# Optimization experiments

Measured on AMD Instinct MI355X. Metric: run time of the kernel, lower is better.

Reference implementation:

```python
import jax, jax.numpy as jnp
import numpy as np
from jax import lax

B, S, H, W = 64, 256, 512, 512


def _lstm_cell(x_t, h, c, Wih, Whh, bih, bhh):
    # PyTorch LSTMCell gate order: i, f, g, o
    g = x_t @ Wih.T + h @ Whh.T + bih + bhh  # [B, 4H]
    i, f, gg, o = jnp.split(g, 4, axis=-1)
    c_new = jax.nn.sigmoid(f) * c + jax.nn.sigmoid(i) * jnp.tanh(gg)
    h_new = jax.nn.sigmoid(o) * jnp.tanh(c_new)
    return h_new, c_new


def setup_inputs() -> dict:
    key = jax.random.key(0)
    ks = jax.random.split(key, 12)
    bnd = 1.0 / np.sqrt(H)
    u = lambda k, shape, b: jax.random.uniform(k, shape, jnp.float32, -b, b)
    return {
        "x": jax.random.normal(ks[0], (B, S, S), jnp.float32),
        "enc_Wih": u(ks[1], (4 * H, S), bnd),
        "enc_Whh": u(ks[2], (4 * H, H), bnd),
        "enc_bih": u(ks[3], (4 * H,), bnd),
        "enc_bhh": u(ks[4], (4 * H,), bnd),
        "dec_Wih": u(ks[5], (4 * H, S), bnd),
        "dec_Whh": u(ks[6], (4 * H, H), bnd),
        "dec_bih": u(ks[7], (4 * H,), bnd),
        "dec_bhh": u(ks[8], (4 * H,), bnd),
        "w1": u(ks[9], (W, H), 1.0 / np.sqrt(H)),
        "w2": u(ks[10], (W, H), 1.0 / np.sqrt(H)),
        "vt": u(ks[11], (W,), 1.0 / np.sqrt(W)),
    }


def reference(x, enc_Wih, enc_Whh, enc_bih, enc_bhh,
              dec_Wih, dec_Whh, dec_bih, dec_bhh, w1, w2, vt):
    xs = x.transpose(1, 0, 2)  # [S, B, S] time-major

    # ---- encoder LSTM (zero initial state, PyTorch default) ----
    def enc_step(carry, x_t):
        h, c = carry
        h, c = _lstm_cell(x_t, h, c, enc_Wih, enc_Whh, enc_bih, enc_bhh)
        return (h, c), h

    h0 = jnp.zeros((B, H), x.dtype)
    (hT, cT), enc_out = lax.scan(enc_step, (h0, h0), xs)  # enc_out: [S, B, H]

    # loop-invariant W1 projection of encoder outputs
    e1 = jnp.einsum('sbh,wh->sbw', enc_out, w1)  # [S, B, W]

    # ---- decoder: hidden updates each step; cell stays at cT (faithful to source) ----
    def dec_step(h, x_t):
        h_new, _ = _lstm_cell(x_t, h, cT, dec_Wih, dec_Whh, dec_bih, dec_bhh)
        att = jnp.tanh(e1 + (h_new @ w2.T)[None, :, :])   # [S, B, W]
        scores = jnp.einsum('sbw,w->sb', att, vt)          # [S, B]
        lp = jax.nn.log_softmax(scores.T, axis=-1)         # [B, S]
        return h_new, lp

    _, probs = lax.scan(dec_step, hT, xs)  # [S_dec, B, S]
    return probs.transpose(1, 0, 2)        # [B, S_dec, S]
```

## Files before the change

### kernel.cpp

```cpp
#include <hip/hip_runtime.h>
#include <cmath>

__device__ __forceinline__ float sigm(float x) { return 1.0f / (1.0f + __expf(-x)); }

__global__ __launch_bounds__(256) void transpose_w(const float* __restrict__ in,
                                                   float* __restrict__ outT, int K) {
  __shared__ float tile[32][33];
  int tx = threadIdx.x & 31, ty = threadIdx.x >> 5;
  int k0 = blockIdx.x * 32;
  int j0 = blockIdx.y * 32;
#pragma unroll
  for (int i = 0; i < 32; i += 8)
    tile[ty + i][tx] = in[(size_t)(j0 + ty + i) * K + k0 + tx];
  __syncthreads();
#pragma unroll
  for (int i = 0; i < 32; i += 8)
    outT[(size_t)(k0 + ty + i) * 2048 + j0 + tx] = tile[tx][ty + i];
}

__device__ __forceinline__ void gemv_j(const float4* __restrict__ A4,
                                       const float4* __restrict__ W4, int j, int kqx,
                                       int kq, int jlo, int jhi, int b0, int b1,
                                       float (&o0)[8], float (&o1)[8]) {
  int qa = (j << 3) + kqx;
  float4 a04 = A4[b0 * 192 + qa];
  float4 a14 = A4[b1 * 192 + qa];
  int wr = ((j << 3) + kq) << 2;
  float a0v[4] = {a04.x, a04.y, a04.z, a04.w};
  float a1v[4] = {a14.x, a14.y, a14.z, a14.w};
#pragma unroll
  for (int i = 0; i < 4; ++i) {
    float4 wlo = W4[(wr + i) * 8 + jlo];
    float4 whi = W4[(wr + i) * 8 + jhi];
    o0[0] = fmaf(a0v[i], wlo.x, o0[0]);
    o0[1] = fmaf(a0v[i], wlo.y, o0[1]);
    o0[2] = fmaf(a0v[i], wlo.z, o0[2]);
    o0[3] = fmaf(a0v[i], wlo.w, o0[3]);
    o0[4] = fmaf(a0v[i], whi.x, o0[4]);
    o0[5] = fmaf(a0v[i], whi.y, o0[5]);
    o0[6] = fmaf(a0v[i], whi.z, o0[6]);
    o0[7] = fmaf(a0v[i], whi.w, o0[7]);
    o1[0] = fmaf(a1v[i], wlo.x, o1[0]);
    o1[1] = fmaf(a1v[i], wlo.y, o1[1]);
    o1[2] = fmaf(a1v[i], wlo.z, o1[2]);
    o1[3] = fmaf(a1v[i], wlo.w, o1[3]);
    o1[4] = fmaf(a1v[i], whi.x, o1[4]);
    o1[5] = fmaf(a1v[i], whi.y, o1[5]);
    o1[6] = fmaf(a1v[i], whi.z, o1[6]);
    o1[7] = fmaf(a1v[i], whi.w, o1[7]);
  }
}

__global__ __launch_bounds__(256, 1) void lstm_chain(
    const float* __restrict__ WT, const float* __restrict__ x,
    const float* __restrict__ bih, const float* __restrict__ bhh,
    float* __restrict__ HBUF,
    float* __restrict__ Cst,
    unsigned int* __restrict__ flg,
    int is_enc) {
  extern __shared__ float lds[];
  float4* W4 = (float4*)lds;
  float4* A4 = (float4*)(lds + 24576);
  float* gates = lds + 24576 + 12288;
  const int bg = blockIdx.x >> 6, ng = blockIdx.x & 63;
  const int tid = threadIdx.x;
  unsigned int* myflag = flg + (size_t)(bg * 64 + ng) * 32;
  unsigned int* dom = flg + (size_t)bg * 64 * 32;

#pragma unroll
  for (int r = 0; r < 24; ++r) {
    int idx = tid + 256 * r;
    int k = idx >> 3, j = idx & 7;
    float4 v =
        *(const float4*)(WT + (size_t)k * 2048 + (j >> 1) * 512 + ng * 8 + (j & 1) * 4);
    W4[k * 8 + (j ^ ((k >> 2) & 7))] = v;
  }
  float bi_i = 0.f, bi_f = 0.f, bi_g = 0.f, bi_o = 0.f, creg = 0.f;
  if (tid < 128) {
    int b = tid >> 3, n8 = tid & 7;
    int n_g = ng * 8 + n8;
    bi_i = bih[n_g] + bhh[n_g];
    bi_f = bih[512 + n_g] + bhh[512 + n_g];
    bi_g = bih[1024 + n_g] + bhh[1024 + n_g];
    bi_o = bih[1536 + n_g] + bhh[1536 + n_g];
    if (!is_enc) creg = Cst[(size_t)(bg * 16 + b) * 512 + n_g];
  }
#pragma unroll
  for (int r = 0; r < 8; ++r) {
    int idx = tid + 256 * r;
    int b = idx >> 7, q = idx & 127;
    float4 v;
    if (is_enc)
      v = make_float4(0.f, 0.f, 0.f, 0.f);
    else
      v = *(const float4*)(HBUF + ((size_t)(255 * 64) + bg * 16 + b) * 512 + 4 * q);
    A4[b * 192 + (q ^ ((b >> 1) & 7))] = v;
  }
#pragma unroll
  for (int r = 0; r < 4; ++r) {
    int idx = tid + 256 * r;
    int b = idx >> 6, q = idx & 63;
    float4 v = *(const float4*)(x + ((size_t)(bg * 16 + b) * 256 + 0) * 256 + 4 * q);
    A4[b * 192 + ((128 + q) ^ ((b >> 1) & 7))] = v;
  }
  __syncthreads();

  const int w = tid >> 6;
  const int lane = tid & 63;
  const int kq = lane >> 3, b8 = lane & 7;
  const int b0 = 2 * b8, b1 = b0 + 1;
  const int jlo = (2 * w) ^ kq, jhi = (2 * w + 1) ^ kq;
  const int kqx = kq ^ b8;

  for (int t = 0; t < 256; ++t) {
    float acc0[8], acc1[8];
#pragma unroll
    for (int g = 0; g < 8; ++g) { acc0[g] = 0.f; acc1[g] = 0.f; }
#pragma unroll 2
    for (int j = 0; j < 24; ++j)
      gemv_j(A4, W4, j, kqx, kq, jlo, jhi, b0, b1, acc0, acc1);
#pragma unroll
    for (int d = 8; d <= 32; d <<= 1) {
#pragma unroll
      for (int g = 0; g < 8; ++g) {
        acc0[g] += __shfl_xor(acc0[g], d, 64);
        acc1[g] += __shfl_xor(acc1[g], d, 64);
      }
    }
    if (kq == 0) {
#pragma unroll
      for (int g = 0; g < 8; ++g) {
        gates[b0 * 40 + w * 8 + g] = acc0[g];
        gates[b1 * 40 + w * 8 + g] = acc1[g];
      }
    }
    __syncthreads();
    if (tid < 128) {
      int b = tid >> 3, n8 = tid & 7;
      float pi = gates[b * 40 + n8] + bi_i;
      float pf = gates[b * 40 + 8 + n8] + bi_f;
      float pg = gates[b * 40 + 16 + n8] + bi_g;
      float po = gates[b * 40 + 24 + n8] + bi_o;
      float ig = sigm(pi), fg = sigm(pf), gg = tanhf(pg), og = sigm(po);
      float cn = fmaf(fg, creg, ig * gg);
      if (is_enc) creg = cn;
      float hn = og * tanhf(cn);
      float* hp = HBUF + ((size_t)t * 64 + bg * 16 + b) * 512 + ng * 8 + n8;
      __hip_atomic_store(hp, hn, __ATOMIC_RELAXED, __HIP_MEMORY_SCOPE_AGENT);
      if (is_enc && t == 255) Cst[(size_t)(bg * 16 + b) * 512 + ng * 8 + n8] = cn;
    }
    if (t == 255) break;
    asm volatile("s_waitcnt vmcnt(0)" ::: "memory");
    __syncthreads();
    if (tid == 0)
      __hip_atomic_store(myflag, (unsigned)(t + 1), __ATOMIC_RELAXED,
                         __HIP_MEMORY_SCOPE_AGENT);
    asm volatile("" ::: "memory");
#pragma unroll
    for (int r = 0; r < 4; ++r) {
      int idx = tid + 256 * r;
      int b = idx >> 6, q = idx & 63;
      float4 v =
          *(const float4*)(x + ((size_t)(bg * 16 + b) * 256 + (t + 1)) * 256 + 4 * q);
      A4[b * 192 + ((128 + q) ^ ((b >> 1) & 7))] = v;
    }
    if (tid < 64) {
      const unsigned tgt = (unsigned)(t + 1);
      unsigned int* fp = dom + (size_t)tid * 32;
      while (true) {
        unsigned v = __hip_atomic_load(fp, __ATOMIC_RELAXED, __HIP_MEMORY_SCOPE_AGENT);
        if (__all((int)(v >= tgt))) break;
        __builtin_amdgcn_s_sleep(1);
      }
    }
    __syncthreads();
    const float4* hb = (const float4*)(HBUF + (size_t)t * 64 * 512);
#pragma unroll
    for (int r = 0; r < 8; ++r) {
      int idx = tid + 256 * r;
      int b = idx >> 7, q = idx & 127;
      float4 v = hb[(size_t)(bg * 16 + b) * 128 + q];
      A4[b * 192 + (q ^ ((b >> 1) & 7))] = v;
    }
    __syncthreads();
  }
}

typedef __attribute__((ext_vector_type(8))) short bf16x8_t;
typedef __attribute__((ext_vector_type(4))) float f32x4_t;

__device__ __forceinline__ unsigned int pack_bf16_rne(float f0, float f1) {
  unsigned int u0 = __float_as_uint(f0);
  unsigned int u1 = __float_as_uint(f1);
  u0 = (u0 + 0x7FFFu + ((u0 >> 16) & 1u)) >> 16;
  u1 = (u1 + 0x7FFFu + ((u1 >> 16) & 1u)) >> 16;
  return u0 | (u1 << 16);
}

__global__ __launch_bounds__(256) void gemm_bf16(const float* __restrict__ A,
                                                 const float* __restrict__ W,
                                                 float* __restrict__ C) {
  __shared__ unsigned short As[128 * 40];
  __shared__ unsigned short Ws[128 * 40];
  int tid = threadIdx.x;
  int n0 = blockIdx.x * 128, m0 = blockIdx.y * 128;
  int wid = tid >> 6, lane = tid & 63;
  int wr = (wid >> 1) * 64, wc = (wid & 1) * 64;
  int l15 = lane & 15, lk = lane >> 4;
  int srow = tid >> 1, shalf = (tid & 1) * 16;
  f32x4_t acc[4][4];
#pragma unroll
  for (int i = 0; i < 4; ++i)
#pragma unroll
    for (int j = 0; j < 4; ++j) acc[i][j] = (f32x4_t){0.f, 0.f, 0.f, 0.f};

  const float* ap = A + (size_t)(m0 + srow) * 512 + shalf;
  const float* wp = W + (size_t)(n0 + srow) * 512 + shalf;

  for (int k0 = 0; k0 < 512; k0 += 32) {
    float4 av0 = *(const float4*)(ap + k0);
    float4 av1 = *(const float4*)(ap + k0 + 4);
    float4 av2 = *(const float4*)(ap + k0 + 8);
    float4 av3 = *(const float4*)(ap + k0 + 12);
    float4 wv0 = *(const float4*)(wp + k0);
    float4 wv1 = *(const float4*)(wp + k0 + 4);
    float4 wv2 = *(const float4*)(wp + k0 + 8);
    float4 wv3 = *(const float4*)(wp + k0 + 12);
    __syncthreads();
    {
      uint4 pa0, pa1, pw0, pw1;
      pa0.x = pack_bf16_rne(av0.x, av0.y);
      pa0.y = pack_bf16_rne(av0.z, av0.w);
      pa0.z = pack_bf16_rne(av1.x, av1.y);
      pa0.w = pack_bf16_rne(av1.z, av1.w);
      pa1.x = pack_bf16_rne(av2.x, av2.y);
      pa1.y = pack_bf16_rne(av2.z, av2.w);
      pa1.z = pack_bf16_rne(av3.x, av3.y);
      pa1.w = pack_bf16_rne(av3.z, av3.w);
      pw0.x = pack_bf16_rne(wv0.x, wv0.y);
      pw0.y = pack_bf16_rne(wv0.z, wv0.w);
      pw0.z = pack_bf16_rne(wv1.x, wv1.y);
      pw0.w = pack_bf16_rne(wv1.z, wv1.w);
      pw1.x = pack_bf16_rne(wv2.x, wv2.y);
      pw1.y = pack_bf16_rne(wv2.z, wv2.w);
      pw1.z = pack_bf16_rne(wv3.x, wv3.y);
      pw1.w = pack_bf16_rne(wv3.z, wv3.w);
      *(uint4*)&As[srow * 40 + shalf] = pa0;
      *(uint4*)&As[srow * 40 + shalf + 8] = pa1;
      *(uint4*)&Ws[srow * 40 + shalf] = pw0;
      *(uint4*)&Ws[srow * 40 + shalf + 8] = pw1;
    }
    __syncthreads();
    bf16x8_t af[4], bf[4];
#pragma unroll
    for (int mi = 0; mi < 4; ++mi)
      af[mi] = *(const bf16x8_t*)&As[(wr + mi * 16 + l15) * 40 + lk * 8];
#pragma unroll
    for (int ni = 0; ni < 4; ++ni)
      bf[ni] = *(const bf16x8_t*)&Ws[(wc + ni * 16 + l15) * 40 + lk * 8];
#pragma unroll
    for (int mi = 0; mi < 4; ++mi)
#pragma unroll
      for (int ni = 0; ni < 4; ++ni)
        acc[mi][ni] = __builtin_amdgcn_mfma_f32_16x16x32_bf16(af[mi], bf[ni],
                                                              acc[mi][ni], 0, 0, 0);
  }
#pragma unroll
  for (int mi = 0; mi < 4; ++mi)
#pragma unroll
    for (int ni = 0; ni < 4; ++ni) {
      float* cp = C + (size_t)(m0 + wr + mi * 16 + lk * 4) * 512 + n0 + wc + ni * 16 + l15;
#pragma unroll
      for (int r = 0; r < 4; ++r) cp[(size_t)r * 512] = acc[mi][ni][r];
    }
}

__global__ __launch_bounds__(256) void scorer(const float* __restrict__ E1,
                                              const float* __restrict__ H2,
                                              const float* __restrict__ vt,
                                              float* __restrict__ out) {
  extern __shared__ float smem[];
  float* e1s = smem;
  float* h2s = smem + 8256;
  const float k2log2e = 2.885390081777927f;
  int tid = threadIdx.x;
  int sx = blockIdx.x;
  int b = blockIdx.y;
#pragma unroll
  for (int j = 0; j < 8; ++j) {
    int idx = tid + 256 * j;
    int r = idx >> 7, c4 = idx & 127;
    float4 v = *(const float4*)(E1 + ((size_t)(sx * 16 + r) * 64 + b) * 512 + c4 * 4);
    *(float4*)&e1s[r * 516 + c4 * 4] = v;
  }
  int tl = tid >> 4, sl = tid & 15;
  for (int tt = 0; tt < 16; ++tt) {
    __syncthreads();
#pragma unroll
    for (int j = 0; j < 8; ++j) {
      int idx = tid + 256 * j;
      int r = idx >> 7, c4 = idx & 127;
      float4 v = *(const float4*)(H2 + ((size_t)(tt * 16 + r) * 64 + b) * 512 + c4 * 4);
      *(float4*)&h2s[r * 516 + c4 * 4] = v;
    }
    __syncthreads();
    float acc = 0.f;
    const float* ep = &e1s[sl * 516];
    const float* hp = &h2s[tl * 516];
#pragma unroll 8
    for (int w4 = 0; w4 < 128; ++w4) {
      float4 a = *(const float4*)(ep + w4 * 4);
      float4 h = *(const float4*)(hp + w4 * 4);
      float4 vv = *(const float4*)(vt + w4 * 4);
      float x0 = a.x + h.x, x1 = a.y + h.y, x2 = a.z + h.z, x3 = a.w + h.w;
      float t0 = fmaf(-2.f, __builtin_amdgcn_rcpf(__builtin_amdgcn_exp2f(x0 * k2log2e) + 1.f), 1.f);
      float t1 = fmaf(-2.f, __builtin_amdgcn_rcpf(__builtin_amdgcn_exp2f(x1 * k2log2e) + 1.f), 1.f);
      float t2 = fmaf(-2.f, __builtin_amdgcn_rcpf(__builtin_amdgcn_exp2f(x2 * k2log2e) + 1.f), 1.f);
      float t3 = fmaf(-2.f, __builtin_amdgcn_rcpf(__builtin_amdgcn_exp2f(x3 * k2log2e) + 1.f), 1.f);
      acc = fmaf(t0, vv.x, acc);
      acc = fmaf(t1, vv.y, acc);
      acc = fmaf(t2, vv.z, acc);
      acc = fmaf(t3, vv.w, acc);
    }
    out[((size_t)b * 256 + tt * 16 + tl) * 256 + sx * 16 + sl] = acc;
  }
}

__global__ __launch_bounds__(256) void logsoftmax_kernel(float* __restrict__ out) {
  __shared__ float red[8];
  int tid = threadIdx.x;
  int wv = tid >> 6, ln = tid & 63;
  float* row = out + (size_t)blockIdx.x * 256;
  float v = row[tid];
  float m = v;
#pragma unroll
  for (int d = 1; d <= 32; d <<= 1) m = fmaxf(m, __shfl_xor(m, d, 64));
  if (ln == 0) red[wv] = m;
  __syncthreads();
  float mx = fmaxf(fmaxf(red[0], red[1]), fmaxf(red[2], red[3]));
  float e = __expf(v - mx);
  float s = e;
#pragma unroll
  for (int d = 1; d <= 32; d <<= 1) s += __shfl_xor(s, d, 64);
  if (ln == 0) red[4 + wv] = s;
  __syncthreads();
  float lse = logf((red[4] + red[5]) + (red[6] + red[7]));
  row[tid] = v - mx - lse;
}

extern "C" void kernel_launch(void* const* d_in, const int* in_sizes, int n_in,
                              void* d_out, int out_size, void* d_ws, size_t ws_size,
                              hipStream_t stream) {
  (void)in_sizes; (void)n_in; (void)out_size; (void)ws_size;
  const float* x = (const float*)d_in[0];
  const float* eWih = (const float*)d_in[1];
  const float* eWhh = (const float*)d_in[2];
  const float* ebih = (const float*)d_in[3];
  const float* ebhh = (const float*)d_in[4];
  const float* dWih = (const float*)d_in[5];
  const float* dWhh = (const float*)d_in[6];
  const float* dbih = (const float*)d_in[7];
  const float* dbhh = (const float*)d_in[8];
  const float* w1 = (const float*)d_in[9];
  const float* w2 = (const float*)d_in[10];
  const float* vt = (const float*)d_in[11];
  float* out = (float*)d_out;
  float* ws = (float*)d_ws;

  float* E1 = ws;
  float* H2 = E1 + 8388608ull;
  float* HBUF = H2 + 8388608ull;
  float* WTe = HBUF + 8388608ull;
  float* WTd = WTe + 1572864ull;
  float* Cst = WTd + 1572864ull;
  unsigned int* FLG = (unsigned int*)(Cst + 32768ull);

  const unsigned ldsB = (24576 + 12288 + 640) * 4;
  const unsigned scorerLds = 2 * 16 * 516 * 4;

  hipMemsetAsync(FLG, 0, 16384 * sizeof(unsigned int), stream);
  transpose_w<<<dim3(16, 64), 256, 0, stream>>>(eWhh, WTe, 512);
  transpose_w<<<dim3(8, 64), 256, 0, stream>>>(eWih, WTe + 512 * 2048, 256);
  transpose_w<<<dim3(16, 64), 256, 0, stream>>>(dWhh, WTd, 512);
  transpose_w<<<dim3(8, 64), 256, 0, stream>>>(dWih, WTd + 512 * 2048, 256);

  {
    const float* a0 = WTe; const float* a1 = x; const float* a2 = ebih;
    const float* a3 = ebhh; float* a4 = HBUF; float* a5 = Cst;
    unsigned int* a6 = FLG; int a7 = 1;
    void* args[] = {&a0, &a1, &a2, &a3, &a4, &a5, &a6, &a7};
    hipLaunchCooperativeKernel((const void*)lstm_chain, dim3(256), dim3(256), args,
                               ldsB, stream);
  }
  gemm_bf16<<<dim3(4, 128), 256, 0, stream>>>(HBUF, w1, E1);
  {
    const float* a0 = WTd; const float* a1 = x; const float* a2 = dbih;
    const float* a3 = dbhh; float* a4 = HBUF; float* a5 = Cst;
    unsigned int* a6 = FLG + 8192; int a7 = 0;
    void* args[] = {&a0, &a1, &a2, &a3, &a4, &a5, &a6, &a7};
    hipLaunchCooperativeKernel((const void*)lstm_chain, dim3(256), dim3(256), args,
                               ldsB, stream);
  }
  gemm_bf16<<<dim3(4, 128), 256, 0, stream>>>(HBUF, w2, H2);
  scorer<<<dim3(16, 64), 256, scorerLds, stream>>>(E1, H2, vt, out);
  logsoftmax_kernel<<<16384, 256, 0, stream>>>(out);
}
```

Measured before the change: 3.813 ms.

## Fuse log-softmax into scorer and merge weight transposes into one launch

The scorer loop is swapped so each block keeps its 16 decoder H2 rows resident and streams all 256 encoder positions of E1. Each thread can then hold a complete 256-wide score row (split across 16 lanes) and apply log-softmax in registers with shuffle reductions, removing the separate logsoftmax kernel and its extra read/write pass over the output. Separately, the four weight-transpose launches are merged into one 3D-grid launch, with the unused blocks for the narrower matrices exiting early. The cost is 16 scores held in registers per thread, and output stores now stride by 16 floats instead of being contiguous.

```diff
diff --git a/kernel.cpp b/kernel.cpp
--- a/kernel.cpp
+++ b/kernel.cpp
@@ -3,11 +3,23 @@
 
 __device__ __forceinline__ float sigm(float x) { return 1.0f / (1.0f + __expf(-x)); }
 
-__global__ __launch_bounds__(256) void transpose_w(const float* __restrict__ in,
-                                                   float* __restrict__ outT, int K) {
+__global__ __launch_bounds__(256) void transpose_all(
+    const float* __restrict__ eWhh, const float* __restrict__ eWih,
+    const float* __restrict__ dWhh, const float* __restrict__ dWih,
+    float* __restrict__ WTe, float* __restrict__ WTd) {
   __shared__ float tile[32][33];
+  const float* in;
+  float* outT;
+  int K;
+  switch (blockIdx.z) {
+    case 0: in = eWhh; outT = WTe; K = 512; break;
+    case 1: in = eWih; outT = WTe + 512 * 2048; K = 256; break;
+    case 2: in = dWhh; outT = WTd; K = 512; break;
+    default: in = dWih; outT = WTd + 512 * 2048; K = 256; break;
+  }
+  int k0 = blockIdx.x * 32;
+  if (k0 >= K) return;
   int tx = threadIdx.x & 31, ty = threadIdx.x >> 5;
-  int k0 = blockIdx.x * 32;
   int j0 = blockIdx.y * 32;
 #pragma unroll
   for (int i = 0; i < 32; i += 8)
@@ -275,33 +287,35 @@
     }
 }
 
-__global__ __launch_bounds__(256) void scorer(const float* __restrict__ E1,
-                                              const float* __restrict__ H2,
-                                              const float* __restrict__ vt,
-                                              float* __restrict__ out) {
+__global__ __launch_bounds__(256) void scorer_fused(const float* __restrict__ E1,
+                                                    const float* __restrict__ H2,
+                                                    const float* __restrict__ vt,
+                                                    float* __restrict__ out) {
   extern __shared__ float smem[];
-  float* e1s = smem;
-  float* h2s = smem + 8256;
+  float* h2s = smem;
+  float* e1s = smem + 8256;
   const float k2log2e = 2.885390081777927f;
   int tid = threadIdx.x;
-  int sx = blockIdx.x;
+  int tx = blockIdx.x;
   int b = blockIdx.y;
 #pragma unroll
   for (int j = 0; j < 8; ++j) {
     int idx = tid + 256 * j;
     int r = idx >> 7, c4 = idx & 127;
-    float4 v = *(const float4*)(E1 + ((size_t)(sx * 16 + r) * 64 + b) * 512 + c4 * 4);
-    *(float4*)&e1s[r * 516 + c4 * 4] = v;
+    float4 v = *(const float4*)(H2 + ((size_t)(tx * 16 + r) * 64 + b) * 512 + c4 * 4);
+    *(float4*)&h2s[r * 516 + c4 * 4] = v;
   }
   int tl = tid >> 4, sl = tid & 15;
-  for (int tt = 0; tt < 16; ++tt) {
+  float score[16];
+#pragma unroll 1
+  for (int ss = 0; ss < 16; ++ss) {
     __syncthreads();
 #pragma unroll
     for (int j = 0; j < 8; ++j) {
       int idx = tid + 256 * j;
       int r = idx >> 7, c4 = idx & 127;
-      float4 v = *(const float4*)(H2 + ((size_t)(tt * 16 + r) * 64 + b) * 512 + c4 * 4);
-      *(float4*)&h2s[r * 516 + c4 * 4] = v;
+      float4 v = *(const float4*)(E1 + ((size_t)(ss * 16 + r) * 64 + b) * 512 + c4 * 4);
+      *(float4*)&e1s[r * 516 + c4 * 4] = v;
     }
     __syncthreads();
     float acc = 0.f;
@@ -322,30 +336,22 @@
       acc = fmaf(t2, vv.z, acc);
       acc = fmaf(t3, vv.w, acc);
     }
-    out[((size_t)b * 256 + tt * 16 + tl) * 256 + sx * 16 + sl] = acc;
-  }
-}
-
-__global__ __launch_bounds__(256) void logsoftmax_kernel(float* __restrict__ out) {
-  __shared__ float red[8];
-  int tid = threadIdx.x;
-  int wv = tid >> 6, ln = tid & 63;
-  float* row = out + (size_t)blockIdx.x * 256;
-  float v = row[tid];
-  float m = v;
-#pragma unroll
-  for (int d = 1; d <= 32; d <<= 1) m = fmaxf(m, __shfl_xor(m, d, 64));
-  if (ln == 0) red[wv] = m;
-  __syncthreads();
-  float mx = fmaxf(fmaxf(red[0], red[1]), fmaxf(red[2], red[3]));
-  float e = __expf(v - mx);
-  float s = e;
-#pragma unroll
-  for (int d = 1; d <= 32; d <<= 1) s += __shfl_xor(s, d, 64);
-  if (ln == 0) red[4 + wv] = s;
-  __syncthreads();
-  float lse = logf((red[4] + red[5]) + (red[6] + red[7]));
-  row[tid] = v - mx - lse;
+    score[ss] = acc;
+  }
+  float mx = score[0];
+#pragma unroll
+  for (int i = 1; i < 16; ++i) mx = fmaxf(mx, score[i]);
+#pragma unroll
+  for (int d = 1; d <= 8; d <<= 1) mx = fmaxf(mx, __shfl_xor(mx, d, 64));
+  float sum = 0.f;
+#pragma unroll
+  for (int i = 0; i < 16; ++i) sum += __expf(score[i] - mx);
+#pragma unroll
+  for (int d = 1; d <= 8; d <<= 1) sum += __shfl_xor(sum, d, 64);
+  float corr = mx + logf(sum);
+  float* rowp = out + ((size_t)b * 256 + tx * 16 + tl) * 256 + sl;
+#pragma unroll
+  for (int ss = 0; ss < 16; ++ss) rowp[ss * 16] = score[ss] - corr;
 }
 
 extern "C" void kernel_launch(void* const* d_in, const int* in_sizes, int n_in,
@@ -379,10 +385,7 @@
   const unsigned scorerLds = 2 * 16 * 516 * 4;
 
   hipMemsetAsync(FLG, 0, 16384 * sizeof(unsigned int), stream);
-  transpose_w<<<dim3(16, 64), 256, 0, stream>>>(eWhh, WTe, 512);
-  transpose_w<<<dim3(8, 64), 256, 0, stream>>>(eWih, WTe + 512 * 2048, 256);
-  transpose_w<<<dim3(16, 64), 256, 0, stream>>>(dWhh, WTd, 512);
-  transpose_w<<<dim3(8, 64), 256, 0, stream>>>(dWih, WTd + 512 * 2048, 256);
+  transpose_all<<<dim3(16, 64, 4), 256, 0, stream>>>(eWhh, eWih, dWhh, dWih, WTe, WTd);
 
   {
     const float* a0 = WTe; const float* a1 = x; const float* a2 = ebih;
@@ -402,6 +405,5 @@
                                ldsB, stream);
   }
   gemm_bf16<<<dim3(4, 128), 256, 0, stream>>>(HBUF, w2, H2);
-  scorer<<<dim3(16, 64), 256, scorerLds, stream>>>(E1, H2, vt, out);
-  logsoftmax_kernel<<<16384, 256, 0, stream>>>(out);
-}
+  scorer_fused<<<dim3(16, 64), 256, scorerLds, stream>>>(E1, H2, vt, out);
+}
```

New measurement: 3.834 ms. Within noise of the previous version (+0.6%).
